# Kernel tuning notes

Measured on AMD Instinct MI355X. Metric: run time of the kernel, lower is better.

Reference implementation:

```python
import jax, jax.numpy as jnp
import numpy as np

NUM_HEADS = 16
HEAD_DIM = 64  # hidden_size 1024 / 16 heads


def setup_inputs() -> dict:
    key = jax.random.key(0)
    k1, k2 = jax.random.split(key)
    B, S, D = 2, 2048, 1024
    hidden_states = jax.random.normal(k1, (B, S, D), dtype=jnp.float32)
    # fast_qkv: bias-free fused qkv projection + separate q/v biases (init zeros in torch)
    W_qkv = jax.random.normal(k2, (D, 3 * D), dtype=jnp.float32) * (1.0 / np.sqrt(D))
    q_bias = jnp.zeros((D,), dtype=jnp.float32)
    v_bias = jnp.zeros((D,), dtype=jnp.float32)
    return {"hidden_states": hidden_states, "W_qkv": W_qkv, "q_bias": q_bias, "v_bias": v_bias}


def reference(hidden_states, W_qkv, q_bias, v_bias):
    B, S, D = hidden_states.shape
    H, hd = NUM_HEADS, HEAD_DIM
    qkv = hidden_states @ W_qkv                      # (B,S,3D)
    q, k, v = jnp.split(qkv, 3, axis=-1)
    q = q + q_bias
    v = v + v_bias
    # (B,S,H,hd)
    q = q.reshape(B, S, H, hd)
    k = k.reshape(B, S, H, hd)
    v = v.reshape(B, S, H, hd)
    q = q / jnp.sqrt(jnp.asarray(hd, dtype=q.dtype))
    # full (B,H,S,S) score tensor, softmax in fp32 then cast back (matches torch)
    scores = jnp.einsum('bqhd,bkhd->bhqk', q, k)
    probs = jax.nn.softmax(scores.astype(jnp.float32), axis=-1).astype(v.dtype)
    ctx = jnp.einsum('bhqk,bkhd->bqhd', probs, v)    # (B,S,H,hd)
    return ctx.reshape(B, S, D)
```

## Files before the change

### kernel.cpp

```cpp
#include <hip/hip_runtime.h>
#include <hip/hip_bf16.h>

typedef _Float16 half_t;
typedef _Float16 h8 __attribute__((ext_vector_type(8)));
typedef _Float16 h4 __attribute__((ext_vector_type(4)));
typedef _Float16 h2 __attribute__((ext_vector_type(2)));
typedef float f32x4 __attribute__((ext_vector_type(4)));
typedef float f4 __attribute__((ext_vector_type(4)));

#define DEVI __device__ __forceinline__

constexpr int NB = 2;
constexpr int S  = 2048;
constexpr int DM = 1024;
constexpr int NH = 16;
constexpr int HD = 64;
constexpr long M = (long)NB * S;
constexpr int N3 = 3 * DM;

DEVI f32x4 mfma16(h8 a, h8 b, f32x4 c) {
  return __builtin_amdgcn_mfma_f32_16x16x32_f16(a, b, c, 0, 0, 0);
}
DEVI f32x4 mfma16h(h4 a, h4 b, f32x4 c) {
  return __builtin_amdgcn_mfma_f32_16x16x16f16(a, b, c, 0, 0, 0);
}
DEVI h8 ld8h(const half_t* p) { return *(const h8*)p; }

#if __has_builtin(__builtin_amdgcn_exp2f)
DEVI float ex2(float x) { return __builtin_amdgcn_exp2f(x); }
#else
DEVI float ex2(float x) { float r; asm("v_exp_f32 %0, %1" : "=v"(r) : "v"(x)); return r; }
#endif

DEVI h2 pk2(float a, float b) {
  auto r = __builtin_amdgcn_cvt_pkrtz(a, b);
  h2 o; __builtin_memcpy(&o, &r, sizeof(o)); return o;
}

DEVI void gl_lds16(const half_t* g, half_t* l) {
  __builtin_amdgcn_global_load_lds(
      (const __attribute__((address_space(1))) void*)g,
      (__attribute__((address_space(3))) void*)l, 16, 0, 0);
}

__global__ void prep(const float* __restrict__ hidden, half_t* __restrict__ Hb,
                     const float* __restrict__ W, half_t* __restrict__ Wt) {
  __shared__ float tile[32][33];
  const int id = blockIdx.x, t = threadIdx.x;
  if (id < 2048) {
    const long i = ((long)id * 256 + t) * 8;
    const f4 a = *(const f4*)(hidden + i), b = *(const f4*)(hidden + i + 4);
    h8 r;
    #pragma unroll
    for (int k = 0; k < 4; k++) { r[k] = (half_t)a[k]; r[4 + k] = (half_t)b[k]; }
    *(h8*)(Hb + i) = r;
  } else {
    const int id2 = id - 2048;
    const int c0 = (id2 % 96) * 32, r0 = (id2 / 96) * 32;
    const int x = t & 31, y = t >> 5;
    #pragma unroll
    for (int i = 0; i < 32; i += 8) tile[y + i][x] = W[(long)(r0 + y + i) * N3 + c0 + x];
    __syncthreads();
    #pragma unroll
    for (int i = 0; i < 32; i += 8)
      Wt[(long)(c0 + y + i) * DM + r0 + x] = (half_t)tile[x][y + i];
  }
}

__global__ __launch_bounds__(256) void qkv_gemm(
    const half_t* __restrict__ A, const half_t* __restrict__ Bt,
    const float* __restrict__ qbias, const float* __restrict__ vbias,
    half_t* __restrict__ Qf, half_t* __restrict__ Kf, half_t* __restrict__ Vt)
{
  constexpr int BM = 128, BN = 128, BK = 32;
  __shared__ alignas(16) half_t As[2][BM * BK];
  __shared__ alignas(16) half_t Bs[2][BN * BK];
  const int t = threadIdx.x, lane = t & 63, wave = t >> 6;
  const int quad = lane >> 4, l16 = lane & 15;
  const int id = blockIdx.x, xcd = id & 7, jj = id >> 3;
  const int m0 = (xcd * 4 + (jj & 3)) * BM;
  const int n0 = (jj >> 2) * BN;
  const int wm = (wave & 1) * 64, wn = (wave >> 1) * 64;

  const half_t* aP0 = A  + (long)(m0 + (t >> 2)) * DM + (t & 3) * 8;
  const half_t* aP1 = aP0 + (long)64 * DM;
  const half_t* bP0 = Bt + (long)(n0 + (t >> 2)) * DM + (t & 3) * 8;
  const half_t* bP1 = bP0 + (long)64 * DM;
  half_t* const asW0 = &As[0][wave * 512];
  half_t* const bsW0 = &Bs[0][wave * 512];
  half_t* const asW1 = &As[1][wave * 512];
  half_t* const bsW1 = &Bs[1][wave * 512];

  f32x4 acc[4][4] = {};

  gl_lds16(aP0, asW0);
  gl_lds16(aP1, asW0 + 2048);
  gl_lds16(bP0, bsW0);
  gl_lds16(bP1, bsW0 + 2048);
  __syncthreads();

  constexpr int NKT = DM / BK;
  for (int kt = 0; kt < NKT; ++kt) {
    const int cur = kt & 1;
    if (kt + 1 < NKT) {
      const int k0 = (kt + 1) * BK;
      gl_lds16(aP0 + k0, cur ? asW0 : asW1);
      gl_lds16(aP1 + k0, (cur ? asW0 : asW1) + 2048);
      gl_lds16(bP0 + k0, cur ? bsW0 : bsW1);
      gl_lds16(bP1 + k0, (cur ? bsW0 : bsW1) + 2048);
    }

    h8 af[4], bfr[4];
    #pragma unroll
    for (int i = 0; i < 4; i++) af[i]  = ld8h(&As[cur][(wm + i * 16 + l16) * BK + quad * 8]);
    #pragma unroll
    for (int j = 0; j < 4; j++) bfr[j] = ld8h(&Bs[cur][(wn + j * 16 + l16) * BK + quad * 8]);
    #pragma unroll
    for (int i = 0; i < 4; i++)
      #pragma unroll
      for (int j = 0; j < 4; j++)
        acc[i][j] = mfma16(af[i], bfr[j], acc[i][j]);

    __syncthreads();
  }

  if (n0 < 2 * DM) {
    #pragma unroll
    for (int i = 0; i < 4; i++) {
      #pragma unroll
      for (int j = 0; j < 4; j++) {
        const int n = n0 + wn + j * 16 + l16;
        #pragma unroll
        for (int r = 0; r < 4; r++) {
          const long m = m0 + wm + i * 16 + quad * 4 + r;
          const float cv = acc[i][j][r];
          if (n < DM) {
            Qf[m * DM + n] = (half_t)((cv + qbias[n]) * 0.1803368801f);
          } else {
            Kf[m * DM + (n - DM)] = (half_t)cv;
          }
        }
      }
    }
  } else {
    const int dBase = n0 + wn - 2 * DM;
    #pragma unroll
    for (int i = 0; i < 4; i++) {
      const long mb = m0 + wm + i * 16 + quad * 4;
      const int bb = (int)(mb >> 11);
      const int ss = (int)(mb & (S - 1));
      #pragma unroll
      for (int j = 0; j < 4; j++) {
        const int dd = dBase + j * 16 + l16;
        const float vb4 = vbias[dd];
        h4 vv;
        #pragma unroll
        for (int r = 0; r < 4; r++) vv[r] = (half_t)(acc[i][j][r] + vb4);
        *(h4*)&Vt[(((long)bb * NH + (dd >> 6)) * HD + (dd & 63)) * S + ss] = vv;
      }
    }
  }
}

__global__ __launch_bounds__(512) void attn(
    const half_t* __restrict__ Qf, const half_t* __restrict__ Kf,
    const half_t* __restrict__ Vt, float* __restrict__ out)
{
  constexpr int LK = 72, LV = 72;
  __shared__ alignas(16) half_t smem[2 * 64 * LK + 2 * 64 * LV];
  half_t* const KsB = smem;
  half_t* const VsB = smem + 2 * 64 * LK;

  const int bh = blockIdx.y, b = bh >> 4, h = bh & 15;
  const int qt = blockIdx.x;
  const int t = threadIdx.x, lane = t & 63, wave = t >> 6;
  const int w4 = wave & 3, kvh = wave >> 2;
  const int quad = lane >> 4, l16 = lane & 15;

  const long qrow0 = (long)b * S + qt * 128 + w4 * 32;
  const half_t* qg = Qf + qrow0 * DM + h * HD;
  const long kb0 = (long)kvh * (S / 2);
  const half_t* kg = Kf + ((long)b * S + kb0) * DM + h * HD;
  const half_t* vg = Vt + (long)bh * HD * S + kb0;

  h8 bq[2][2];
  #pragma unroll
  for (int qi = 0; qi < 2; qi++)
    #pragma unroll
    for (int dh = 0; dh < 2; dh++)
      bq[qi][dh] = ld8h(&qg[(long)(qi * 16 + l16) * DM + dh * 32 + quad * 8]);

  const int tg = t & 255;
  const int r0s = tg >> 3, c0s = (tg & 7) * 8;
  const int r1s = 32 + r0s;
  half_t* const ksW = KsB + kvh * (64 * LK);
  half_t* const vsW = VsB + kvh * (64 * LV);
  h8 kreg[2], vreg[2];
  kreg[0] = ld8h(&kg[(long)r0s * DM + c0s]);
  kreg[1] = ld8h(&kg[(long)r1s * DM + c0s]);
  vreg[0] = ld8h(&vg[(long)r0s * S + c0s]);
  vreg[1] = ld8h(&vg[(long)r1s * S + c0s]);

  const f32x4 z4 = {0.f, 0.f, 0.f, 0.f};
  const h4 vones = {(half_t)1.f, (half_t)1.f, (half_t)1.f, (half_t)1.f};

  f32x4 O[2][4] = {};
  f32x4 lacc[2] = {};

  constexpr int NT = (S / 2) / 64;
  for (int kt = 0; kt < NT; ++kt) {
    __syncthreads();
    *(h8*)&ksW[r0s * LK + c0s] = kreg[0];
    *(h8*)&ksW[r1s * LK + c0s] = kreg[1];
    *(h8*)&vsW[r0s * LV + c0s] = vreg[0];
    *(h8*)&vsW[r1s * LV + c0s] = vreg[1];
    __syncthreads();

    if (kt < NT - 1) {
      const long ko = (long)(kt + 1) * 64;
      kreg[0] = ld8h(&kg[(ko + r0s) * DM + c0s]);
      kreg[1] = ld8h(&kg[(ko + r1s) * DM + c0s]);
      vreg[0] = ld8h(&vg[(long)r0s * S + ko + c0s]);
      vreg[1] = ld8h(&vg[(long)r1s * S + ko + c0s]);
    }

    h4 pa[2][4];
    #pragma unroll
    for (int g = 0; g < 4; g++) {
      const h8 kf0 = ld8h(&ksW[(g * 16 + l16) * LK + quad * 8]);
      const h8 kf1 = ld8h(&ksW[(g * 16 + l16) * LK + 32 + quad * 8]);
      #pragma unroll
      for (int qi = 0; qi < 2; qi++) {
        f32x4 sc = mfma16(kf0, bq[qi][0], z4);
        sc = mfma16(kf1, bq[qi][1], sc);
        const h2 lo = pk2(ex2(sc[0]), ex2(sc[1]));
        const h2 hi = pk2(ex2(sc[2]), ex2(sc[3]));
        union { h4 v; h2 p[2]; } u; u.p[0] = lo; u.p[1] = hi;
        pa[qi][g] = u.v;
      }
    }

    #pragma unroll
    for (int g = 0; g < 4; g++) {
      lacc[0] = mfma16h(pa[0][g], vones, lacc[0]);
      lacc[1] = mfma16h(pa[1][g], vones, lacc[1]);
    }

    #pragma unroll
    for (int j = 0; j < 4; j++) {
      #pragma unroll
      for (int g = 0; g < 4; g++) {
        const h4 vf = *(const h4*)&vsW[(j * 16 + l16) * LV + g * 16 + quad * 4];
        O[0][j] = mfma16h(pa[0][g], vf, O[0][j]);
        O[1][j] = mfma16h(pa[1][g], vf, O[1][j]);
      }
    }
  }

  __syncthreads();
  float* const xb = (float*)smem;
  float* const xl = xb + 8192;
  if (kvh) {
    #pragma unroll
    for (int qi = 0; qi < 2; qi++) {
      #pragma unroll
      for (int j = 0; j < 4; j++)
        *(f4*)&xb[(((w4 * 2 + qi) * 4 + j) * 64 + lane) * 4] = O[qi][j];
      if (l16 == 0) {
        #pragma unroll
        for (int r = 0; r < 4; r++)
          xl[(w4 * 2 + qi) * 16 + quad * 4 + r] = lacc[qi][r];
      }
    }
  }
  __syncthreads();
  if (!kvh) {
    #pragma unroll
    for (int qi = 0; qi < 2; qi++) {
      #pragma unroll
      for (int j = 0; j < 4; j++)
        O[qi][j] += *(const f4*)&xb[(((w4 * 2 + qi) * 4 + j) * 64 + lane) * 4];
      #pragma unroll
      for (int r = 0; r < 4; r++) {
        const float linv = 1.f / (lacc[qi][r] + xl[(w4 * 2 + qi) * 16 + quad * 4 + r]);
        const long srow = qrow0 + qi * 16 + quad * 4 + r;
        #pragma unroll
        for (int j = 0; j < 4; j++)
          out[srow * DM + h * HD + j * 16 + l16] = O[qi][j][r] * linv;
      }
    }
  }
}

extern "C" void kernel_launch(void* const* d_in, const int* in_sizes, int n_in,
                              void* d_out, int out_size, void* d_ws, size_t ws_size,
                              hipStream_t stream) {
  (void)in_sizes; (void)n_in; (void)out_size; (void)ws_size;
  const float* hidden = (const float*)d_in[0];
  const float* W      = (const float*)d_in[1];
  const float* qbias  = (const float*)d_in[2];
  const float* vbias  = (const float*)d_in[3];
  float* out = (float*)d_out;

  half_t* ws = (half_t*)d_ws;
  half_t* Hb = ws;
  half_t* Wt = Hb + M * DM;
  half_t* Qf = Wt + (long)N3 * DM;
  half_t* Kf = Qf + M * DM;
  half_t* Vt = Kf + M * DM;

  prep<<<2048 + 3072, 256, 0, stream>>>(hidden, Hb, W, Wt);
  qkv_gemm<<<(N3 / 128) * (int)(M / 128), 256, 0, stream>>>(Hb, Wt, qbias, vbias, Qf, Kf, Vt);
  attn<<<dim3(S / 128, NB * NH), 512, 0, stream>>>(Qf, Kf, Vt, out);
}
```

Baseline: 175.4 us.

## Triple-buffer QKV GEMM LDS loads with partial vmcnt waits

Moves the QKV projection GEMM from double to triple buffering in LDS, so loads are issued two k-tiles ahead. The full __syncthreads is replaced with s_waitcnt vmcnt(4) plus a raw barrier, which lets the next tile's global-to-LDS loads stay in flight while the current tile is computed. The intent is to hide global memory latency better. The cost is 50% more LDS per block, which may lower occupancy. The hand-written waitcnt also depends on exactly four loads being issued per stage.

```diff
diff --git a/kernel.cpp b/kernel.cpp
--- a/kernel.cpp
+++ b/kernel.cpp
@@ -73,8 +73,8 @@
     half_t* __restrict__ Qf, half_t* __restrict__ Kf, half_t* __restrict__ Vt)
 {
   constexpr int BM = 128, BN = 128, BK = 32;
-  __shared__ alignas(16) half_t As[2][BM * BK];
-  __shared__ alignas(16) half_t Bs[2][BN * BK];
+  __shared__ alignas(16) half_t As[3][BM * BK];
+  __shared__ alignas(16) half_t Bs[3][BN * BK];
   const int t = threadIdx.x, lane = t & 63, wave = t >> 6;
   const int quad = lane >> 4, l16 = lane & 15;
   const int id = blockIdx.x, xcd = id & 7, jj = id >> 3;
@@ -86,28 +86,33 @@
   const half_t* aP1 = aP0 + (long)64 * DM;
   const half_t* bP0 = Bt + (long)(n0 + (t >> 2)) * DM + (t & 3) * 8;
   const half_t* bP1 = bP0 + (long)64 * DM;
-  half_t* const asW0 = &As[0][wave * 512];
-  half_t* const bsW0 = &Bs[0][wave * 512];
-  half_t* const asW1 = &As[1][wave * 512];
-  half_t* const bsW1 = &Bs[1][wave * 512];
+  const int wb = wave * 512;
 
   f32x4 acc[4][4] = {};
 
-  gl_lds16(aP0, asW0);
-  gl_lds16(aP1, asW0 + 2048);
-  gl_lds16(bP0, bsW0);
-  gl_lds16(bP1, bsW0 + 2048);
-  __syncthreads();
+  {
+    gl_lds16(aP0, &As[0][wb]);
+    gl_lds16(aP1, &As[0][wb] + 2048);
+    gl_lds16(bP0, &Bs[0][wb]);
+    gl_lds16(bP1, &Bs[0][wb] + 2048);
+    gl_lds16(aP0 + BK, &As[1][wb]);
+    gl_lds16(aP1 + BK, &As[1][wb] + 2048);
+    gl_lds16(bP0 + BK, &Bs[1][wb]);
+    gl_lds16(bP1 + BK, &Bs[1][wb] + 2048);
+    asm volatile("s_waitcnt vmcnt(4)" ::: "memory");
+    __builtin_amdgcn_sched_barrier(0);
+    __builtin_amdgcn_s_barrier();
+  }
 
   constexpr int NKT = DM / BK;
   for (int kt = 0; kt < NKT; ++kt) {
-    const int cur = kt & 1;
-    if (kt + 1 < NKT) {
-      const int k0 = (kt + 1) * BK;
-      gl_lds16(aP0 + k0, cur ? asW0 : asW1);
-      gl_lds16(aP1 + k0, (cur ? asW0 : asW1) + 2048);
-      gl_lds16(bP0 + k0, cur ? bsW0 : bsW1);
-      gl_lds16(bP1 + k0, (cur ? bsW0 : bsW1) + 2048);
+    const int cur = kt % 3;
+    if (kt + 2 < NKT) {
+      const int nsl = (kt + 2) % 3, k0 = (kt + 2) * BK;
+      gl_lds16(aP0 + k0, &As[nsl][wb]);
+      gl_lds16(aP1 + k0, &As[nsl][wb] + 2048);
+      gl_lds16(bP0 + k0, &Bs[nsl][wb]);
+      gl_lds16(bP1 + k0, &Bs[nsl][wb] + 2048);
     }
 
     h8 af[4], bfr[4];
@@ -121,7 +126,12 @@
       for (int j = 0; j < 4; j++)
         acc[i][j] = mfma16(af[i], bfr[j], acc[i][j]);
 
-    __syncthreads();
+    if (kt + 1 < NKT) {
+      if (kt + 2 < NKT) asm volatile("s_waitcnt vmcnt(4)" ::: "memory");
+      else              asm volatile("s_waitcnt vmcnt(0)" ::: "memory");
+      __builtin_amdgcn_sched_barrier(0);
+      __builtin_amdgcn_s_barrier();
+    }
   }
 
   if (n0 < 2 * DM) {
```

After: 176.3 us. Within noise of the previous version (+0.5%).
